# Kernel optimization log

Hardware: AMD Instinct MI355X
Metric: run time of the kernel (lower is better)

## Reference

```python
import jax, jax.numpy as jnp
import numpy as np

N = 100000      # num_nodes
E = 1600000     # num edges (avg degree 16)
R = 400         # num_relations passed to GCNLayer (masks at R and 2R)
DIN, DH, DOUT = 128, 128, 128
EPS = 1e-5


def setup_inputs() -> dict:
    key = jax.random.key(0)
    ks = jax.random.split(key, 8)
    src = jax.random.randint(ks[0], (E,), 0, N)
    dst = jax.random.randint(ks[1], (E,), 0, N)
    rel = jax.random.randint(ks[2], (E,), 0, 2 * R + 1)  # covers orig/inverse/self-loop buckets
    edges = jnp.stack([src, rel, dst], axis=1)  # [E,3] = (head, rel, tail)

    def xinit(k, shape, fan_in):
        return jax.random.normal(k, shape, jnp.float32) * (1.0 / np.sqrt(fan_in))

    node_emb = xinit(ks[3], (N, DIN), DIN)
    # stacked relation-branch linears: [3, out, in] = (original, inverse, self_loop)
    W1 = xinit(ks[4], (3, DH, DIN), DIN)
    b1 = jnp.zeros((3, DH), jnp.float32)
    Ws1 = xinit(ks[5], (DH, DIN), DIN)
    bs1 = jnp.zeros((DH,), jnp.float32)
    g1 = jnp.ones((DH,), jnp.float32)
    be1 = jnp.zeros((DH,), jnp.float32)
    W2 = xinit(ks[6], (3, DOUT, DH), DH)
    b2 = jnp.zeros((3, DOUT), jnp.float32)
    Ws2 = xinit(ks[7], (DOUT, DH), DH)
    bs2 = jnp.zeros((DOUT,), jnp.float32)
    g2 = jnp.ones((DOUT,), jnp.float32)
    be2 = jnp.zeros((DOUT,), jnp.float32)
    return dict(edges=edges, node_emb=node_emb, W1=W1, b1=b1, Ws1=Ws1, bs1=bs1,
                g1=g1, be1=be1, W2=W2, b2=b2, Ws2=Ws2, bs2=bs2, g2=g2, be2=be2)


def _gcn_layer(x, src, dst, bucket, W, b):
    # Project node features once per relation branch (same math as projecting
    # gathered src features, but N << E so this is cheaper): Y[r] = x @ W[r].T + b[r]
    Y = jnp.einsum('nd,rod->rno', x, W) + b[:, None, :]     # [3, N, out]
    msgs = Y[bucket, src]                                   # [E, out] gather by (branch, src)
    n = x.shape[0]
    out = jax.ops.segment_sum(msgs, dst, num_segments=n)    # scatter-add to dst
    cnt = jax.ops.segment_sum(jnp.ones_like(dst, dtype=x.dtype), dst, num_segments=n)
    out = out / jnp.maximum(cnt, 1.0)[:, None]              # degree norm, clamp min=1
    return jax.nn.relu(out)


def _layer_norm(x, g, b):
    m = jnp.mean(x, axis=-1, keepdims=True)
    v = jnp.mean((x - m) ** 2, axis=-1, keepdims=True)
    return (x - m) * jax.lax.rsqrt(v + EPS) * g + b


def reference(edges, node_emb, W1, b1, Ws1, bs1, g1, be1, W2, b2, Ws2, bs2, g2, be2):
    src, rel, dst = edges[:, 0], edges[:, 1], edges[:, 2]
    # bucket: 0=original (rel<R), 1=inverse (R<=rel<2R), 2=self-loop (rel>=2R)
    bucket = (rel >= R).astype(jnp.int32) + (rel >= 2 * R).astype(jnp.int32)

    x1 = _gcn_layer(node_emb, src, dst, bucket, W1, b1)
    x1 = x1 + node_emb @ Ws1.T + bs1                # skip1
    x1 = _layer_norm(x1, g1, be1)                   # dropout: eval-mode identity

    x2 = _gcn_layer(x1, src, dst, bucket, W2, b2)
    x2 = x2 + x1 @ Ws2.T + bs2                      # skip2
    x2 = _layer_norm(x2, g2, be2)
    return x2
```

## Files before the change

### kernel.cpp

```cpp
#include <hip/hip_runtime.h>
#include <stdint.h>

typedef unsigned int uint;
typedef unsigned short ushort;

#define NNODES 100000
#define NPAD   100096
#define NEDGES 1600000
#define RCONST 400
#define CAP    64

#define NBKT   196
#define NBLK_A 512
#define EPB    3125
#define RUNCAP 64

typedef __attribute__((ext_vector_type(8))) short short8;
typedef __attribute__((ext_vector_type(4))) float f32x4;

__device__ __forceinline__ float bflo(uint u){ union{uint i;float f;}c; c.i=u<<16; return c.f; }
__device__ __forceinline__ float bfhi(uint u){ union{uint i;float f;}c; c.i=u&0xFFFF0000u; return c.f; }
__device__ __forceinline__ ushort f2bf(float f){ union{uint i;float ff;}c; c.ff=f; uint u=c.i;
    return (ushort)((u + 0x7FFFu + ((u>>16)&1u))>>16); }
__device__ __forceinline__ uint pack2(float lo, float hi){
    return (uint)f2bf(lo) | ((uint)f2bf(hi)<<16); }


__global__ __launch_bounds__(256) void binfill_kernel(const int* __restrict__ edges,
                                                      int* __restrict__ runcnt,
                                                      uint* __restrict__ binned) {
    __shared__ int pos[NBKT];
    int blk = blockIdx.x, tid = threadIdx.x;
    for (int i = tid; i < NBKT; i += 256) pos[i] = 0;
    __syncthreads();
    int start = blk * EPB;
    for (int i = tid; i < EPB; i += 256) {
        int e = start + i;
        int src = edges[e * 3];
        int rel = edges[e * 3 + 1];
        int dst = edges[e * 3 + 2];
        int bkt = (rel >= RCONST) + (rel >= 2 * RCONST);
        int b = dst >> 9, off = dst & 511;
        int p = atomicAdd(&pos[b], 1);
        if (p < RUNCAP)
            binned[((size_t)b * NBLK_A + blk) * RUNCAP + p] =
                (uint)src | ((uint)bkt << 17) | ((uint)off << 19);
    }
    __syncthreads();
    for (int i = tid; i < NBKT; i += 256)
        runcnt[blk * NBKT + i] = min(pos[i], RUNCAP);
}


__global__ __launch_bounds__(256) void scatter_kernel(const uint* __restrict__ binned,
                                                      const int* __restrict__ runcnt,
                                                      int* __restrict__ cnt,
                                                      int* __restrict__ elist) {
    __shared__ int c512[512];
    int b = blockIdx.x, tid = threadIdx.x;
    int base = b << 9;
    for (int i = tid; i < 512; i += 256) c512[i] = 0;
    __syncthreads();
    #pragma unroll
    for (int rr = 0; rr < 2; ++rr) {
        int r = tid * 2 + rr;
        int n = runcnt[r * NBKT + b];
        const uint* p = binned + ((size_t)b * NBLK_A + r) * RUNCAP;
        for (int i = 0; i < n; ++i) {
            uint e = p[i];
            int off = (int)(e >> 19);
            int q = atomicAdd(&c512[off], 1);
            if (q < CAP) elist[(size_t)(base + off) * CAP + q] = (int)(e & 0x7FFFFu);
        }
    }
    __syncthreads();
    for (int i = tid; i < 512; i += 256) {
        int node = base + i;
        if (node < NPAD) cnt[node] = min(c512[i], CAP);
    }
}


__global__ __launch_bounds__(256) void convx_kernel(const float* __restrict__ x,
                                                    uint* __restrict__ xb) {
    size_t i = (size_t)blockIdx.x * 256 + threadIdx.x;
    if (i < (size_t)NNODES * 64) {
        float2 f = *(const float2*)&x[i * 2];
        xb[i] = pack2(f.x, f.y);
    }
}

__global__ __launch_bounds__(256) void wconv_kernel(const float* __restrict__ W,
                                                    const float* __restrict__ Ws,
                                                    uint* __restrict__ Wb) {
    int i = blockIdx.x * 256 + threadIdx.x;
    if (i < 128 * 256) {
        int n = i >> 8, kp = i & 255, k = kp * 2;
        float v0, v1;
        if (k < 384) {
            int r = k >> 7, kk = k & 127;
            const float* p = W + r * 16384 + n * 128 + kk;
            v0 = p[0]; v1 = p[1];
        } else {
            const float* p = Ws + n * 128 + (k - 384);
            v0 = p[0]; v1 = p[1];
        }
        Wb[i] = pack2(v0, v1);
    }
}


__global__ __launch_bounds__(256) void gather_kernel(
    const uint* __restrict__ xb,
    const int* __restrict__ cnt,
    const int* __restrict__ elist,
    uint* __restrict__ Ab,
    float4* __restrict__ cnts) {
    int w = threadIdx.x >> 6, lane = threadIdx.x & 63;
    int node = blockIdx.x * 4 + w;
    int deg = min(cnt[node], CAP);
    float inv = 1.0f / fmaxf((float)deg, 1.0f);

    float a0l = 0.f, a0h = 0.f, a1l = 0.f, a1h = 0.f, a2l = 0.f, a2h = 0.f;
    int c0 = 0, c1 = 0, c2 = 0;

    for (int base = 0; base < deg; base += 64) {
        int m = min(64, deg - base);
        int ve = 0;
        if (lane < m) ve = elist[(size_t)node * CAP + base + lane];

        int j = 0;
        for (; j + 4 <= m; j += 4) {
            int e0 = __builtin_amdgcn_readlane(ve, j);
            int e1 = __builtin_amdgcn_readlane(ve, j + 1);
            int e2 = __builtin_amdgcn_readlane(ve, j + 2);
            int e3 = __builtin_amdgcn_readlane(ve, j + 3);
            int s0 = e0 & 0x1FFFF, k0 = e0 >> 17;
            int s1 = e1 & 0x1FFFF, k1 = e1 >> 17;
            int s2 = e2 & 0x1FFFF, k2 = e2 >> 17;
            int s3 = e3 & 0x1FFFF, k3 = e3 >> 17;
            uint u0 = xb[((size_t)s0 << 6) + lane];
            uint u1 = xb[((size_t)s1 << 6) + lane];
            uint u2 = xb[((size_t)s2 << 6) + lane];
            uint u3 = xb[((size_t)s3 << 6) + lane];

            float q00 = (k0 == 0) ? 1.f : 0.f, q01 = (k0 == 1) ? 1.f : 0.f, q02 = (k0 == 2) ? 1.f : 0.f;
            float q10 = (k1 == 0) ? 1.f : 0.f, q11 = (k1 == 1) ? 1.f : 0.f, q12 = (k1 == 2) ? 1.f : 0.f;
            float q20 = (k2 == 0) ? 1.f : 0.f, q21 = (k2 == 1) ? 1.f : 0.f, q22 = (k2 == 2) ? 1.f : 0.f;
            float q30 = (k3 == 0) ? 1.f : 0.f, q31 = (k3 == 1) ? 1.f : 0.f, q32 = (k3 == 2) ? 1.f : 0.f;
            c0 += (k0 == 0) + (k1 == 0) + (k2 == 0) + (k3 == 0);
            c1 += (k0 == 1) + (k1 == 1) + (k2 == 1) + (k3 == 1);
            c2 += (k0 == 2) + (k1 == 2) + (k2 == 2) + (k3 == 2);

            float f0l = bflo(u0), f0h = bfhi(u0);
            float f1l = bflo(u1), f1h = bfhi(u1);
            float f2l = bflo(u2), f2h = bfhi(u2);
            float f3l = bflo(u3), f3h = bfhi(u3);

            a0l = fmaf(q00, f0l, a0l); a1l = fmaf(q01, f0l, a1l); a2l = fmaf(q02, f0l, a2l);
            a0h = fmaf(q00, f0h, a0h); a1h = fmaf(q01, f0h, a1h); a2h = fmaf(q02, f0h, a2h);
            a0l = fmaf(q10, f1l, a0l); a1l = fmaf(q11, f1l, a1l); a2l = fmaf(q12, f1l, a2l);
            a0h = fmaf(q10, f1h, a0h); a1h = fmaf(q11, f1h, a1h); a2h = fmaf(q12, f1h, a2h);
            a0l = fmaf(q20, f2l, a0l); a1l = fmaf(q21, f2l, a1l); a2l = fmaf(q22, f2l, a2l);
            a0h = fmaf(q20, f2h, a0h); a1h = fmaf(q21, f2h, a1h); a2h = fmaf(q22, f2h, a2h);
            a0l = fmaf(q30, f3l, a0l); a1l = fmaf(q31, f3l, a1l); a2l = fmaf(q32, f3l, a2l);
            a0h = fmaf(q30, f3h, a0h); a1h = fmaf(q31, f3h, a1h); a2h = fmaf(q32, f3h, a2h);
        }
        for (; j < m; ++j) {
            int ee = __builtin_amdgcn_readlane(ve, j);
            int s = ee & 0x1FFFF, k = ee >> 17;
            uint u = xb[((size_t)s << 6) + lane];
            float q0 = (k == 0) ? 1.f : 0.f;
            float q1 = (k == 1) ? 1.f : 0.f;
            float q2 = (k == 2) ? 1.f : 0.f;
            c0 += (k == 0); c1 += (k == 1); c2 += (k == 2);
            float fl = bflo(u), fh = bfhi(u);
            a0l = fmaf(q0, fl, a0l); a1l = fmaf(q1, fl, a1l); a2l = fmaf(q2, fl, a2l);
            a0h = fmaf(q0, fh, a0h); a1h = fmaf(q1, fh, a1h); a2h = fmaf(q2, fh, a2h);
        }
    }

    size_t ab = (size_t)node * 192 + lane;
    Ab[ab]       = pack2(a0l * inv, a0h * inv);
    Ab[ab + 64]  = pack2(a1l * inv, a1h * inv);
    Ab[ab + 128] = pack2(a2l * inv, a2h * inv);
    if (lane == 0) {
        float4 v; v.x = (float)c0; v.y = (float)c1; v.z = (float)c2; v.w = inv;
        cnts[node] = v;
    }
}


template<bool OUT_BF16>
__global__ __launch_bounds__(256, 2) void gemm_kernel(
    const ushort* __restrict__ Ab,
    const ushort* __restrict__ xb,
    const ushort* __restrict__ Wb,
    const float* __restrict__ bia,
    const float* __restrict__ bs,
    const float* __restrict__ g,
    const float* __restrict__ be,
    const float4* __restrict__ cnts,
    void* __restrict__ out) {
    __shared__ char smem[128 * 136 * 2 * 2];
    __shared__ float sMean[128], sRstd[128];
    ushort (*lA)[136] = (ushort(*)[136])smem;
    ushort (*lB)[136] = (ushort(*)[136])(smem + 128 * 136 * 2);
    float  (*vt)[132] = (float(*)[132])smem;

    int tid = threadIdx.x;
    int w = tid >> 6, lane = tid & 63;
    int wm = w >> 1, wn = w & 1;
    int quad = lane >> 4, l15 = lane & 15;
    int node0 = blockIdx.x * 128;

    f32x4 accm[4][4], accq[4][4];
    f32x4 zero = {0.f, 0.f, 0.f, 0.f};
    #pragma unroll
    for (int i = 0; i < 4; ++i)
        #pragma unroll
        for (int j = 0; j < 4; ++j) { accm[i][j] = zero; accq[i][j] = zero; }

    for (int kc = 0; kc < 4; ++kc) {
        const ushort* srcA; int strA;
        if (kc < 3) { srcA = Ab + (size_t)node0 * 384 + kc * 128; strA = 384; }
        else        { srcA = xb + (size_t)node0 * 128;            strA = 128; }
        const ushort* srcB = Wb + kc * 128;
        __syncthreads();
        #pragma unroll
        for (int i = 0; i < 8; ++i) {
            int li = i * 256 + tid;
            int row = li >> 4, cs = li & 15;
            *(uint4*)&lA[row][cs * 8] = *(const uint4*)(srcA + (size_t)row * strA + cs * 8);
            *(uint4*)&lB[row][cs * 8] = *(const uint4*)(srcB + (size_t)row * 512  + cs * 8);
        }
        __syncthreads();
        #pragma unroll
        for (int ks = 0; ks < 4; ++ks) {
            short8 aF[4], bF[4];
            #pragma unroll
            for (int mt = 0; mt < 4; ++mt)
                aF[mt] = *(const short8*)&lA[wm * 64 + mt * 16 + l15][ks * 32 + quad * 8];
            #pragma unroll
            for (int nt = 0; nt < 4; ++nt)
                bF[nt] = *(const short8*)&lB[wn * 64 + nt * 16 + l15][ks * 32 + quad * 8];
            if (kc < 3) {
                #pragma unroll
                for (int mt = 0; mt < 4; ++mt)
                    #pragma unroll
                    for (int nt = 0; nt < 4; ++nt)
                        accm[mt][nt] = __builtin_amdgcn_mfma_f32_16x16x32_bf16(
                            aF[mt], bF[nt], accm[mt][nt], 0, 0, 0);
            } else {
                #pragma unroll
                for (int mt = 0; mt < 4; ++mt)
                    #pragma unroll
                    for (int nt = 0; nt < 4; ++nt)
                        accq[mt][nt] = __builtin_amdgcn_mfma_f32_16x16x32_bf16(
                            aF[mt], bF[nt], accq[mt][nt], 0, 0, 0);
            }
        }
    }

    __syncthreads();
    #pragma unroll
    for (int mt = 0; mt < 4; ++mt) {
        #pragma unroll
        for (int r = 0; r < 4; ++r) {
            int ml = wm * 64 + mt * 16 + quad * 4 + r;
            float4 c4 = cnts[node0 + ml];
            #pragma unroll
            for (int nt = 0; nt < 4; ++nt) {
                int nl = wn * 64 + nt * 16 + l15;
                float bd = (c4.x * bia[nl] + c4.y * bia[128 + nl] + c4.z * bia[256 + nl]) * c4.w;
                float mval = accm[mt][nt][r] + bd;
                float v = fmaxf(mval, 0.f) + accq[mt][nt][r] + bs[nl];
                vt[ml][nl] = v;
            }
        }
    }
    __syncthreads();
    if (tid < 128) {
        float s1 = 0.f, s2 = 0.f;
        const float* row = vt[tid];
        #pragma unroll 8
        for (int c = 0; c < 128; c += 4) {
            float4 a = *(const float4*)&row[c];
            s1 += (a.x + a.y) + (a.z + a.w);
            s2 += (a.x * a.x + a.y * a.y) + (a.z * a.z + a.w * a.w);
        }
        float mean = s1 * (1.f / 128.f);
        float var = s2 * (1.f / 128.f) - mean * mean;
        sMean[tid] = mean;
        sRstd[tid] = rsqrtf(var + 1e-5f);
    }
    __syncthreads();
    if (OUT_BF16) {
        uint* o = (uint*)out;
        for (int idx = tid; idx < 128 * 64; idx += 256) {
            int row = idx >> 6, cp = idx & 63;
            int node = node0 + row;
            if (node < NNODES) {
                float mn = sMean[row], rs = sRstd[row];
                int c0 = cp * 2;
                float v0 = (vt[row][c0] - mn) * rs * g[c0] + be[c0];
                float v1 = (vt[row][c0 + 1] - mn) * rs * g[c0 + 1] + be[c0 + 1];
                o[(size_t)node * 64 + cp] = pack2(v0, v1);
            }
        }
    } else {
        float* o = (float*)out;
        for (int idx = tid; idx < 128 * 128; idx += 256) {
            int row = idx >> 7, col = idx & 127;
            int node = node0 + row;
            if (node < NNODES)
                o[(size_t)node * 128 + col] =
                    (vt[row][col] - sMean[row]) * sRstd[row] * g[col] + be[col];
        }
    }
}


extern "C" void kernel_launch(void* const* d_in, const int* in_sizes, int n_in,
                              void* d_out, int out_size, void* d_ws, size_t ws_size,
                              hipStream_t stream) {
    (void)in_sizes; (void)n_in; (void)out_size; (void)ws_size;

    const int*   edges = (const int*)d_in[0];
    const float* xemb  = (const float*)d_in[1];
    const float* W1  = (const float*)d_in[2];
    const float* b1  = (const float*)d_in[3];
    const float* Ws1 = (const float*)d_in[4];
    const float* bs1 = (const float*)d_in[5];
    const float* g1  = (const float*)d_in[6];
    const float* be1 = (const float*)d_in[7];
    const float* W2  = (const float*)d_in[8];
    const float* b2  = (const float*)d_in[9];
    const float* Ws2 = (const float*)d_in[10];
    const float* bs2 = (const float*)d_in[11];
    const float* g2  = (const float*)d_in[12];
    const float* be2 = (const float*)d_in[13];

    char* ws = (char*)d_ws;
    auto take = [&](size_t bytes) {
        char* p = ws;
        ws += (bytes + 255) & ~(size_t)255;
        return p;
    };
    int*    cnt    = (int*)take((size_t)NPAD * 4);
    int*    elist  = (int*)take((size_t)NPAD * CAP * 4);
    float4* cnts   = (float4*)take((size_t)NPAD * 16);
    uint*   xb0    = (uint*)take((size_t)NPAD * 128 * 2);
    uint*   xb1    = (uint*)take((size_t)NPAD * 128 * 2);
    uint*   Ab     = (uint*)take((size_t)NPAD * 384 * 2);
    uint*   Wb1    = (uint*)take((size_t)128 * 512 * 2);
    uint*   Wb2    = (uint*)take((size_t)128 * 512 * 2);
    int*    runcnt = (int*)take((size_t)NBLK_A * NBKT * 4);
    uint*   binned = (uint*)take((size_t)NBKT * NBLK_A * RUNCAP * 4);

    binfill_kernel<<<NBLK_A, 256, 0, stream>>>(edges, runcnt, binned);
    scatter_kernel<<<NBKT, 256, 0, stream>>>(binned, runcnt, cnt, elist);

    convx_kernel<<<(NNODES * 64) / 256, 256, 0, stream>>>(xemb, xb0);
    wconv_kernel<<<128, 256, 0, stream>>>(W1, Ws1, Wb1);
    wconv_kernel<<<128, 256, 0, stream>>>(W2, Ws2, Wb2);

    gather_kernel<<<NNODES / 4, 256, 0, stream>>>(xb0, cnt, elist, Ab, cnts);
    gemm_kernel<true><<<(NNODES + 127) / 128, 256, 0, stream>>>(
        (const ushort*)Ab, (const ushort*)xb0, (const ushort*)Wb1,
        b1, bs1, g1, be1, cnts, xb1);

    gather_kernel<<<NNODES / 4, 256, 0, stream>>>(xb1, cnt, elist, Ab, cnts);
    gemm_kernel<false><<<(NNODES + 127) / 128, 256, 0, stream>>>(
        (const ushort*)Ab, (const ushort*)xb1, (const ushort*)Wb2,
        b2, bs2, g2, be2, cnts, d_out);
}
```

Before: 453.1 us.

## Load GEMM fragments directly from global memory and fuse LayerNorm via shuffles

The fused GEMM+LayerNorm kernel no longer stages A and W tiles through LDS. Each of 8 waves (512 threads, a 2x4 wave grid) loads its MFMA fragments straight from global memory. Row sums for LayerNorm are reduced with lane shuffles plus a small shared partial array, and results are normalized and written from registers instead of through an LDS transpose tile. This removes LDS traffic and barriers and raises waves per block. The cost is uncoalesced 16-byte strided global reads and redundant reads of A across the wn waves, relying on cache.

```diff
diff --git a/kernel.cpp b/kernel.cpp
--- a/kernel.cpp
+++ b/kernel.cpp
@@ -192,7 +192,7 @@
 
 
 template<bool OUT_BF16>
-__global__ __launch_bounds__(256, 2) void gemm_kernel(
+__global__ __launch_bounds__(512, 2) void gemm_kernel(
     const ushort* __restrict__ Ab,
     const ushort* __restrict__ xb,
     const ushort* __restrict__ Wb,
@@ -202,120 +202,127 @@
     const float* __restrict__ be,
     const float4* __restrict__ cnts,
     void* __restrict__ out) {
-    __shared__ char smem[128 * 136 * 2 * 2];
+    __shared__ float sS1[4][128], sS2[4][128];
     __shared__ float sMean[128], sRstd[128];
-    ushort (*lA)[136] = (ushort(*)[136])smem;
-    ushort (*lB)[136] = (ushort(*)[136])(smem + 128 * 136 * 2);
-    float  (*vt)[132] = (float(*)[132])smem;
 
     int tid = threadIdx.x;
     int w = tid >> 6, lane = tid & 63;
-    int wm = w >> 1, wn = w & 1;
+    int wm = w >> 2, wn = w & 3;
     int quad = lane >> 4, l15 = lane & 15;
     int node0 = blockIdx.x * 128;
 
-    f32x4 accm[4][4], accq[4][4];
+    f32x4 accm[4][2], accq[4][2];
     f32x4 zero = {0.f, 0.f, 0.f, 0.f};
     #pragma unroll
     for (int i = 0; i < 4; ++i)
         #pragma unroll
-        for (int j = 0; j < 4; ++j) { accm[i][j] = zero; accq[i][j] = zero; }
-
-    for (int kc = 0; kc < 4; ++kc) {
-        const ushort* srcA; int strA;
-        if (kc < 3) { srcA = Ab + (size_t)node0 * 384 + kc * 128; strA = 384; }
-        else        { srcA = xb + (size_t)node0 * 128;            strA = 128; }
-        const ushort* srcB = Wb + kc * 128;
-        __syncthreads();
-        #pragma unroll
-        for (int i = 0; i < 8; ++i) {
-            int li = i * 256 + tid;
-            int row = li >> 4, cs = li & 15;
-            *(uint4*)&lA[row][cs * 8] = *(const uint4*)(srcA + (size_t)row * strA + cs * 8);
-            *(uint4*)&lB[row][cs * 8] = *(const uint4*)(srcB + (size_t)row * 512  + cs * 8);
-        }
-        __syncthreads();
+        for (int j = 0; j < 2; ++j) { accm[i][j] = zero; accq[i][j] = zero; }
+
+    const ushort* pA = Ab + (size_t)(node0 + wm * 64 + l15) * 384 + quad * 8;
+    const ushort* pX = xb + (size_t)(node0 + wm * 64 + l15) * 128 + quad * 8;
+    const ushort* pB = Wb + (size_t)(wn * 32 + l15) * 512 + quad * 8;
+
+    #pragma unroll
+    for (int kc = 0; kc < 3; ++kc) {
         #pragma unroll
         for (int ks = 0; ks < 4; ++ks) {
-            short8 aF[4], bF[4];
+            int ko = kc * 128 + ks * 32;
+            short8 aF[4], bF[2];
             #pragma unroll
             for (int mt = 0; mt < 4; ++mt)
-                aF[mt] = *(const short8*)&lA[wm * 64 + mt * 16 + l15][ks * 32 + quad * 8];
-            #pragma unroll
-            for (int nt = 0; nt < 4; ++nt)
-                bF[nt] = *(const short8*)&lB[wn * 64 + nt * 16 + l15][ks * 32 + quad * 8];
-            if (kc < 3) {
+                aF[mt] = *(const short8*)(pA + (size_t)mt * 16 * 384 + ko);
+            #pragma unroll
+            for (int nt = 0; nt < 2; ++nt)
+                bF[nt] = *(const short8*)(pB + (size_t)nt * 16 * 512 + ko);
+            #pragma unroll
+            for (int mt = 0; mt < 4; ++mt)
                 #pragma unroll
-                for (int mt = 0; mt < 4; ++mt)
-                    #pragma unroll
-                    for (int nt = 0; nt < 4; ++nt)
-                        accm[mt][nt] = __builtin_amdgcn_mfma_f32_16x16x32_bf16(
-                            aF[mt], bF[nt], accm[mt][nt], 0, 0, 0);
-            } else {
-                #pragma unroll
-                for (int mt = 0; mt < 4; ++mt)
-                    #pragma unroll
-                    for (int nt = 0; nt < 4; ++nt)
-                        accq[mt][nt] = __builtin_amdgcn_mfma_f32_16x16x32_bf16(
-                            aF[mt], bF[nt], accq[mt][nt], 0, 0, 0);
-            }
-        }
-    }
-
-    __syncthreads();
+                for (int nt = 0; nt < 2; ++nt)
+                    accm[mt][nt] = __builtin_amdgcn_mfma_f32_16x16x32_bf16(
+                        aF[mt], bF[nt], accm[mt][nt], 0, 0, 0);
+        }
+    }
+    #pragma unroll
+    for (int ks = 0; ks < 4; ++ks) {
+        int xo = ks * 32, ko = 384 + ks * 32;
+        short8 aF[4], bF[2];
+        #pragma unroll
+        for (int mt = 0; mt < 4; ++mt)
+            aF[mt] = *(const short8*)(pX + (size_t)mt * 16 * 128 + xo);
+        #pragma unroll
+        for (int nt = 0; nt < 2; ++nt)
+            bF[nt] = *(const short8*)(pB + (size_t)nt * 16 * 512 + ko);
+        #pragma unroll
+        for (int mt = 0; mt < 4; ++mt)
+            #pragma unroll
+            for (int nt = 0; nt < 2; ++nt)
+                accq[mt][nt] = __builtin_amdgcn_mfma_f32_16x16x32_bf16(
+                    aF[mt], bF[nt], accq[mt][nt], 0, 0, 0);
+    }
+
+    int nl0 = wn * 32 + l15;
+    float pb0[2], pb1[2], pb2[2], pbs[2], pg[2], pbe[2];
+    #pragma unroll
+    for (int nt = 0; nt < 2; ++nt) {
+        int nl = nl0 + nt * 16;
+        pb0[nt] = bia[nl]; pb1[nt] = bia[128 + nl]; pb2[nt] = bia[256 + nl];
+        pbs[nt] = bs[nl];  pg[nt] = g[nl];          pbe[nt] = be[nl];
+    }
     #pragma unroll
     for (int mt = 0; mt < 4; ++mt) {
         #pragma unroll
         for (int r = 0; r < 4; ++r) {
             int ml = wm * 64 + mt * 16 + quad * 4 + r;
             float4 c4 = cnts[node0 + ml];
-            #pragma unroll
-            for (int nt = 0; nt < 4; ++nt) {
-                int nl = wn * 64 + nt * 16 + l15;
-                float bd = (c4.x * bia[nl] + c4.y * bia[128 + nl] + c4.z * bia[256 + nl]) * c4.w;
-                float mval = accm[mt][nt][r] + bd;
-                float v = fmaxf(mval, 0.f) + accq[mt][nt][r] + bs[nl];
-                vt[ml][nl] = v;
+            float s1 = 0.f, s2 = 0.f;
+            #pragma unroll
+            for (int nt = 0; nt < 2; ++nt) {
+                float bd = (c4.x * pb0[nt] + c4.y * pb1[nt] + c4.z * pb2[nt]) * c4.w;
+                float v = fmaxf(accm[mt][nt][r] + bd, 0.f) + accq[mt][nt][r] + pbs[nt];
+                accm[mt][nt][r] = v;
+                s1 += v; s2 += v * v;
             }
+            #pragma unroll
+            for (int mask = 1; mask < 16; mask <<= 1) {
+                s1 += __shfl_xor(s1, mask);
+                s2 += __shfl_xor(s2, mask);
+            }
+            if (l15 == 0) { sS1[wn][ml] = s1; sS2[wn][ml] = s2; }
         }
     }
     __syncthreads();
     if (tid < 128) {
-        float s1 = 0.f, s2 = 0.f;
-        const float* row = vt[tid];
-        #pragma unroll 8
-        for (int c = 0; c < 128; c += 4) {
-            float4 a = *(const float4*)&row[c];
-            s1 += (a.x + a.y) + (a.z + a.w);
-            s2 += (a.x * a.x + a.y * a.y) + (a.z * a.z + a.w * a.w);
-        }
+        float s1 = sS1[0][tid] + sS1[1][tid] + sS1[2][tid] + sS1[3][tid];
+        float s2 = sS2[0][tid] + sS2[1][tid] + sS2[2][tid] + sS2[3][tid];
         float mean = s1 * (1.f / 128.f);
         float var = s2 * (1.f / 128.f) - mean * mean;
         sMean[tid] = mean;
         sRstd[tid] = rsqrtf(var + 1e-5f);
     }
     __syncthreads();
-    if (OUT_BF16) {
-        uint* o = (uint*)out;
-        for (int idx = tid; idx < 128 * 64; idx += 256) {
-            int row = idx >> 6, cp = idx & 63;
-            int node = node0 + row;
-            if (node < NNODES) {
-                float mn = sMean[row], rs = sRstd[row];
-                int c0 = cp * 2;
-                float v0 = (vt[row][c0] - mn) * rs * g[c0] + be[c0];
-                float v1 = (vt[row][c0 + 1] - mn) * rs * g[c0 + 1] + be[c0 + 1];
-                o[(size_t)node * 64 + cp] = pack2(v0, v1);
+    #pragma unroll
+    for (int mt = 0; mt < 4; ++mt) {
+        #pragma unroll
+        for (int r = 0; r < 4; ++r) {
+            int ml = wm * 64 + mt * 16 + quad * 4 + r;
+            int node = node0 + ml;
+            float mn = sMean[ml], rs = sRstd[ml];
+            #pragma unroll
+            for (int nt = 0; nt < 2; ++nt) {
+                float v = (accm[mt][nt][r] - mn) * rs * pg[nt] + pbe[nt];
+                if (OUT_BF16) {
+                    float vh = __shfl_xor(v, 1);
+                    if (!(l15 & 1) && node < NNODES) {
+                        uint* o = (uint*)out;
+                        o[(size_t)node * 64 + wn * 16 + nt * 8 + (l15 >> 1)] = pack2(v, vh);
+                    }
+                } else {
+                    if (node < NNODES) {
+                        float* o = (float*)out;
+                        o[(size_t)node * 128 + nl0 + nt * 16] = v;
+                    }
+                }
             }
-        }
-    } else {
-        float* o = (float*)out;
-        for (int idx = tid; idx < 128 * 128; idx += 256) {
-            int row = idx >> 7, col = idx & 127;
-            int node = node0 + row;
-            if (node < NNODES)
-                o[(size_t)node * 128 + col] =
-                    (vt[row][col] - sMean[row]) * sRstd[row] * g[col] + be[col];
         }
     }
 }
@@ -366,12 +373,12 @@
     wconv_kernel<<<128, 256, 0, stream>>>(W2, Ws2, Wb2);
 
     gather_kernel<<<NNODES / 4, 256, 0, stream>>>(xb0, cnt, elist, Ab, cnts);
-    gemm_kernel<true><<<(NNODES + 127) / 128, 256, 0, stream>>>(
+    gemm_kernel<true><<<(NNODES + 127) / 128, 512, 0, stream>>>(
         (const ushort*)Ab, (const ushort*)xb0, (const ushort*)Wb1,
         b1, bs1, g1, be1, cnts, xb1);
 
     gather_kernel<<<NNODES / 4, 256, 0, stream>>>(xb1, cnt, elist, Ab, cnts);
-    gemm_kernel<false><<<(NNODES + 127) / 128, 256, 0, stream>>>(
+    gemm_kernel<false><<<(NNODES + 127) / 128, 512, 0, stream>>>(
         (const ushort*)Ab, (const ushort*)xb1, (const ushort*)Wb2,
         b2, bs2, g2, be2, cnts, d_out);
 }
```

Measured after the change: 526.3 us. 1.16x slower.
